# Performance work log

Measured on AMD Instinct MI355X. Metric: run time of the kernel, lower is better.

The kernel has to match this reference:

```python
import jax, jax.numpy as jnp
import numpy as np
import math

MAX_L = 3
N_RBF = 8
CUTOFF = 5.5
P_CUT = 6
ZS = (1, 6, 7, 8)
N_NODES = 10000
N_EDGES = 60000
N_EMB = 3  # n_atom_basis; edge channels = N_EMB**2 = 9


def _lxlylz_list(max_l):
    lst = []
    for l in range(max_l + 1):
        for lx in range(l, -1, -1):
            for ly in range(l - lx, -1, -1):
                lst.append((lx, ly, l - lx - ly))
    return lst

LXLYLZ = _lxlylz_list(MAX_L)            # 20 monomial exponent triples
IDX = {v: i for i, v in enumerate(LXLYLZ)}
L_OF = np.array([sum(v) for v in LXLYLZ], dtype=np.int32)
LX = jnp.array([v[0] for v in LXLYLZ])
LY = jnp.array([v[1] for v in LXLYLZ])
LZ = jnp.array([v[2] for v in LXLYLZ])
L_OF_J = jnp.array(L_OF)
ZS_J = jnp.array(ZS)


def _multinom(v):
    l = sum(v)
    return math.factorial(l) // (math.factorial(v[0]) * math.factorial(v[1]) * math.factorial(v[2]))


def _splits(l):
    return [v for v in LXLYLZ if sum(v) == l]


def _nu2_terms():
    # B2_l = sum_{|lvec|=l} multinom(lvec) * A_lvec^2  (contraction of (r1.r2)^l)
    out = []
    for l in range(1, MAX_L + 1):
        vs = _splits(l)
        idx = jnp.array([IDX[v] for v in vs])
        pref = jnp.array([float(_multinom(v)) for v in vs], dtype=jnp.float32)
        out.append((idx, idx, pref))
    return out


def _nu3_terms():
    # invariants from (r1.r2)^e12 (r1.r3)^e13 (r2.r3)^e23, all e>=1, vector degrees <= MAX_L
    combos = [(a, b, c) for a in range(1, MAX_L + 1) for b in range(1, MAX_L + 1)
              for c in range(1, MAX_L + 1) if a + b <= MAX_L and a + c <= MAX_L and b + c <= MAX_L]
    out = []
    for (e12, e13, e23) in combos:
        coef = {}
        for va in _splits(e12):
            for vb in _splits(e13):
                for vc in _splits(e23):
                    v1 = (va[0] + vb[0], va[1] + vb[1], va[2] + vb[2])
                    v2 = (va[0] + vc[0], va[1] + vc[1], va[2] + vc[2])
                    v3 = (vb[0] + vc[0], vb[1] + vc[1], vb[2] + vc[2])
                    key = (v1, v2, v3)
                    coef[key] = coef.get(key, 0.0) + float(_multinom(va) * _multinom(vb) * _multinom(vc))
        keys = list(coef.keys())
        i1 = jnp.array([IDX[k[0]] for k in keys])
        i2 = jnp.array([IDX[k[1]] for k in keys])
        i3 = jnp.array([IDX[k[2]] for k in keys])
        pref = jnp.array([coef[k] for k in keys], dtype=jnp.float32)
        out.append((i1, i2, i3, pref))
    return out

NU2_TERMS = _nu2_terms()
NU3_TERMS = _nu3_terms()


def setup_inputs() -> dict:
    key = jax.random.key(0)
    k1, k2, k3, k4, k5 = jax.random.split(key, 5)
    positions = jax.random.uniform(k1, (N_NODES, 3), dtype=jnp.float32) * 4.0  # box so most r < cutoff
    atomic_numbers = ZS_J[jax.random.randint(k2, (N_NODES,), 0, len(ZS))]
    edge_index = jax.random.randint(k3, (2, N_EDGES), 0, N_NODES)
    shifts = jnp.zeros((N_EDGES, 3), jnp.float32)
    embedding_weight = jax.random.normal(k4, (len(ZS), N_EMB), jnp.float32) / np.sqrt(len(ZS))
    radial_weight = jax.random.normal(k5, (MAX_L + 1, N_RBF, N_RBF), jnp.float32) / np.sqrt(N_RBF)
    return {"positions": positions, "shifts": shifts, "embedding_weight": embedding_weight,
            "radial_weight": radial_weight, "atomic_numbers": atomic_numbers, "edge_index": edge_index}


def reference(positions, shifts, embedding_weight, radial_weight, atomic_numbers, edge_index):
    # node one-hot + embedding
    onehot = (atomic_numbers[:, None] == ZS_J[None, :]).astype(positions.dtype)
    emb = onehot @ embedding_weight                                   # [N, n_emb]
    snd, rcv = edge_index[0], edge_index[1]
    E = snd.shape[0]
    # directed edge encoding: outer product of endpoint embeddings -> [E, n_emb^2]
    enc = (emb[snd][:, :, None] * emb[rcv][:, None, :]).reshape(E, -1)
    # edge vectors / lengths (normalized)
    vec = positions[rcv] - positions[snd] + shifts
    length = jnp.maximum(jnp.linalg.norm(vec, axis=-1, keepdims=True), 1e-9)  # [E,1]
    unit = vec / length
    # Bessel RBF * polynomial cutoff
    n = jnp.arange(1, N_RBF + 1, dtype=positions.dtype)
    rbf = jnp.sqrt(2.0 / CUTOFF) * jnp.sin(n * jnp.pi * length / CUTOFF) / length  # [E,R]
    x = length / CUTOFF
    p = float(P_CUT)
    fc = (1.0 - 0.5 * (p + 1) * (p + 2) * x ** P_CUT + p * (p + 2) * x ** (P_CUT + 1)
          - 0.5 * p * (p + 1) * x ** (P_CUT + 2)) * (x < 1.0)
    radial = rbf * fc                                                  # [E,R]
    # angular monomials x^lx y^ly z^lz
    pw = unit[:, :, None] ** jnp.arange(MAX_L + 1)                     # [E,3,L+1]
    ang = pw[:, 0, LX] * pw[:, 1, LY] * pw[:, 2, LZ]                   # [E,A=20]
    # triple outer product -> per-edge attribute tensor [E,R,A,C]
    edge_attr = jnp.einsum('er,ea,ec->erac', radial, ang, enc)
    # shared per-l radial linear transform
    Wa = radial_weight[L_OF_J]                                         # [A,R,R]
    edge_attr = jnp.einsum('ars,erac->esac', Wa, edge_attr)
    # scatter-sum to receiver nodes -> A basis
    A = jax.ops.segment_sum(edge_attr, rcv, num_segments=positions.shape[0])  # [N,R,A,C]
    # symmetrizer: invariant B basis up to nu=3
    feats = [A[:, :, 0, :]]                                            # nu=1: A_{000}
    for i1, i2, pref in NU2_TERMS:
        feats.append(jnp.einsum('t,nrtc->nrc', pref, A[:, :, i1, :] * A[:, :, i2, :]))
    for i1, i2, i3, pref in NU3_TERMS:
        feats.append(jnp.einsum('t,nrtc->nrc', pref, A[:, :, i1, :] * A[:, :, i2, :] * A[:, :, i3, :]))
    return jnp.stack(feats, axis=2)                                    # [N, R, n_B=8, C]
```

## Files before the change

### kernel.cpp

```cpp
#include <hip/hip_runtime.h>

constexpr int NRBF = 8;
constexpr int NA   = 20;
constexpr int NC   = 9;
constexpr int EDW  = 64;
constexpr int CAP  = 64;

__constant__ int cLX[NA] = {0,1,0,0,2,1,1,0,0,0,3,2,2,1,1,1,0,0,0,0};
__constant__ int cLY[NA] = {0,0,1,0,0,1,0,2,1,0,0,1,0,2,1,0,3,2,1,0};
__constant__ int cLZ[NA] = {0,0,0,1,0,0,1,0,1,2,0,0,1,0,1,2,0,1,2,3};
__constant__ int cLOF[NA]= {0,1,1,1,2,2,2,2,2,2,3,3,3,3,3,3,3,3,3,3};

__device__ __forceinline__ int zmap(int z) {
    return z == 1 ? 0 : (z == 6 ? 1 : (z == 7 ? 2 : 3));
}

struct Nu3Tbl {
    int n;
    unsigned char i1[200], i2[200], i3[200], cb[200];
    float pref[200];
};
constexpr int idx_of(int lx, int ly, int lz) {
    int l = lx + ly + lz;
    int base = (l == 0) ? 0 : ((l == 1) ? 1 : ((l == 2) ? 4 : 10));
    int d = l - lx;
    return base + d * (d + 1) / 2 + (d - ly);
}
constexpr int factc(int k) { return k <= 1 ? 1 : k * factc(k - 1); }
constexpr float multinom(int lx, int ly, int lz) {
    return (float)(factc(lx + ly + lz) / (factc(lx) * factc(ly) * factc(lz)));
}
constexpr Nu3Tbl make_nu3() {
    Nu3Tbl t{};
    const int combos[4][3] = {{1,1,1},{1,1,2},{1,2,1},{2,1,1}};
    for (int q = 0; q < 4; ++q) {
        int e12 = combos[q][0], e13 = combos[q][1], e23 = combos[q][2];
        for (int ax = e12; ax >= 0; --ax) for (int ay = e12-ax; ay >= 0; --ay) { int az = e12-ax-ay;
        for (int bx = e13; bx >= 0; --bx) for (int by = e13-bx; by >= 0; --by) { int bz = e13-bx-by;
        for (int cx = e23; cx >= 0; --cx) for (int cy = e23-cx; cy >= 0; --cy) { int cz = e23-cx-cy;
            t.i1[t.n] = (unsigned char)idx_of(ax+bx, ay+by, az+bz);
            t.i2[t.n] = (unsigned char)idx_of(ax+cx, ay+cy, az+cz);
            t.i3[t.n] = (unsigned char)idx_of(bx+cx, by+cy, bz+cz);
            t.cb[t.n] = (unsigned char)q;
            t.pref[t.n] = multinom(ax,ay,az) * multinom(bx,by,bz) * multinom(cx,cy,cz);
            t.n++;
        }}}
    }
    return t;
}
constexpr Nu3Tbl NU3 = make_nu3();

__global__ __launch_bounds__(256) void precompute_kernel(
    const float* __restrict__ pos, const float* __restrict__ shifts,
    const float* __restrict__ embW, const float* __restrict__ radW,
    const int* __restrict__ zs, const int* __restrict__ eidx,
    float* __restrict__ edata, int* __restrict__ counts, int* __restrict__ order,
    int E)
{
    __shared__ float s_rad[4][NRBF];
    int w = threadIdx.x >> 6;
    int lane = threadIdx.x & 63;
    int e = blockIdx.x * 4 + w;
    bool valid = (e < E);

    int snd = 0, rcv = 0;
    float dx = 0.f, dy = 0.f, dz = 0.f, len = 1.f;
    if (valid) {
        snd = eidx[e]; rcv = eidx[E + e];
        dx = pos[rcv*3+0] - pos[snd*3+0] + shifts[e*3+0];
        dy = pos[rcv*3+1] - pos[snd*3+1] + shifts[e*3+1];
        dz = pos[rcv*3+2] - pos[snd*3+2] + shifts[e*3+2];
        len = fmaxf(sqrtf(dx*dx + dy*dy + dz*dz), 1e-9f);
    }
    if (valid && lane < 8) {
        float x = len * (1.0f / 5.5f);
        float fc = 0.f;
        if (x < 1.f) {
            float x2 = x * x, x6 = x2 * x2 * x2;
            fc = 1.f - 28.f * x6 + 48.f * x6 * x - 21.f * x6 * x2;
        }
        float rbf = 0.60302268915552724f *
                    sinf((float)(lane + 1) * 3.14159265358979323846f * len / 5.5f) / len;
        s_rad[w][lane] = rbf * fc;
    }
    __syncthreads();
    if (valid) {
        float v = 0.f;
        if (lane < 32) {
            int l = lane >> 3, s = lane & 7;
            float acc = 0.f;
            #pragma unroll
            for (int r = 0; r < 8; ++r) acc += radW[(l * 8 + r) * 8 + s] * s_rad[w][r];
            v = acc;
        } else if (lane < 52) {
            int a = lane - 32;
            float inv = 1.f / len;
            float ux = dx * inv, uy = dy * inv, uz = dz * inv;
            float t = 1.f;
            for (int k = 0; k < cLX[a]; ++k) t *= ux;
            for (int k = 0; k < cLY[a]; ++k) t *= uy;
            for (int k = 0; k < cLZ[a]; ++k) t *= uz;
            v = t;
        } else if (lane < 61) {
            int t = lane - 52;
            v = embW[zmap(zs[snd]) * 3 + t / 3] * embW[zmap(zs[rcv]) * 3 + t % 3];
        }
        edata[(size_t)e * EDW + lane] = v;
        if (lane == 0) {
            int p = atomicAdd(&counts[rcv], 1);
            if (p < CAP) order[rcv * CAP + p] = e;
        }
    }
}

__global__ __launch_bounds__(256) void node_kernel(
    const float* __restrict__ edata, const int* __restrict__ counts,
    const int* __restrict__ order, float* __restrict__ out, int N)
{
    int n = blockIdx.x;
    if (n >= N) return;
    __shared__ float ed[4][EDW];
    __shared__ float A[NRBF * NA * NC];
    __shared__ float Bsh[NRBF * 8 * NC];
    int tid = threadIdx.x;
    int deg = min(counts[n], CAP);

    bool active = (tid < NRBF * NA);
    int s_i = tid / NA, a_i = tid % NA;
    int roff = active ? (cLOF[a_i] * 8 + s_i) : 0;
    int goff = 32 + a_i;
    float acc[NC];
    #pragma unroll
    for (int c = 0; c < NC; ++c) acc[c] = 0.f;

    for (int j = 0; j < deg; j += 4) {
        int slot = tid >> 6, elem = tid & 63;
        if (j + slot < deg)
            ed[slot][elem] = edata[(size_t)order[n * CAP + j + slot] * EDW + elem];
        __syncthreads();
        int m_end = min(4, deg - j);
        for (int m = 0; m < m_end; ++m) {
            if (active) {
                float p = ed[m][roff] * ed[m][goff];
                #pragma unroll
                for (int c = 0; c < NC; ++c) acc[c] += p * ed[m][52 + c];
            }
        }
        __syncthreads();
    }

    if (active) {
        int base = (s_i * NA + a_i) * NC;
        #pragma unroll
        for (int c = 0; c < NC; ++c) A[base + c] = acc[c];
    }
    __syncthreads();

    if (tid < 72) {
        int s = tid / 9, c = tid % 9;
        float Av[NA];
        #pragma unroll
        for (int a = 0; a < NA; ++a) Av[a] = A[(s * NA + a) * NC + c];

        float b0 = Av[0];
        float b1 = Av[1]*Av[1] + Av[2]*Av[2] + Av[3]*Av[3];
        float b2 = Av[4]*Av[4] + 2.f*Av[5]*Av[5] + 2.f*Av[6]*Av[6]
                 + Av[7]*Av[7] + 2.f*Av[8]*Av[8] + Av[9]*Av[9];
        float b3 = Av[10]*Av[10] + 3.f*(Av[11]*Av[11] + Av[12]*Av[12] + Av[13]*Av[13])
                 + 6.f*Av[14]*Av[14] + 3.f*Av[15]*Av[15] + Av[16]*Av[16]
                 + 3.f*(Av[17]*Av[17] + Av[18]*Av[18]) + Av[19]*Av[19];
        float b4 = 0.f, b5 = 0.f, b6 = 0.f, b7 = 0.f;
        #pragma unroll
        for (int k = 0; k < NU3.n; ++k) {
            float term = NU3.pref[k] * Av[NU3.i1[k]] * Av[NU3.i2[k]] * Av[NU3.i3[k]];
            if      (NU3.cb[k] == 0) b4 += term;
            else if (NU3.cb[k] == 1) b5 += term;
            else if (NU3.cb[k] == 2) b6 += term;
            else                     b7 += term;
        }
        int sb = s * 8 * NC + c;
        Bsh[sb + 0*NC] = b0; Bsh[sb + 1*NC] = b1; Bsh[sb + 2*NC] = b2; Bsh[sb + 3*NC] = b3;
        Bsh[sb + 4*NC] = b4; Bsh[sb + 5*NC] = b5; Bsh[sb + 6*NC] = b6; Bsh[sb + 7*NC] = b7;
    }
    __syncthreads();
    float* op = out + (size_t)n * (NRBF * 8 * NC);
    for (int i = tid; i < NRBF * 8 * NC; i += 256) op[i] = Bsh[i];
}

extern "C" void kernel_launch(void* const* d_in, const int* in_sizes, int n_in,
                              void* d_out, int out_size, void* d_ws, size_t ws_size,
                              hipStream_t stream) {
    const float* pos    = (const float*)d_in[0];
    const float* shifts = (const float*)d_in[1];
    const float* embW   = (const float*)d_in[2];
    const float* radW   = (const float*)d_in[3];
    const int*   zs     = (const int*)d_in[4];
    const int*   eidx   = (const int*)d_in[5];
    float* out = (float*)d_out;

    int N = in_sizes[0] / 3;
    int E = in_sizes[5] / 2;

    float* edata = (float*)d_ws;
    int* counts  = (int*)(edata + (size_t)E * EDW);
    int* order   = counts + N;

    hipMemsetAsync(counts, 0, (size_t)N * sizeof(int), stream);

    precompute_kernel<<<dim3((E + 3) / 4), dim3(256), 0, stream>>>(
        pos, shifts, embW, radW, zs, eidx, edata, counts, order, E);

    node_kernel<<<dim3(N), dim3(256), 0, stream>>>(edata, counts, order, out, N);
}
```

Baseline: 134.9 us.

## Remap node kernel threads to (rbf, channel) owning all 20 monomials

The node kernel now assigns each of 72 threads one (radial, channel) pair that accumulates all 20 angular components in registers. This removes the shared-memory A staging and the extra barrier before the symmetrizer. Edges are staged 16 at a time instead of 4, and the block shrinks to 128 threads, which cuts synchronisations and the number of idle threads. In exchange, fewer threads do more serial work per edge and register pressure goes up.

```diff
diff --git a/kernel.cpp b/kernel.cpp
--- a/kernel.cpp
+++ b/kernel.cpp
@@ -5,11 +5,13 @@
 constexpr int NC   = 9;
 constexpr int EDW  = 64;
 constexpr int CAP  = 64;
+constexpr int STG  = 16;
 
 __constant__ int cLX[NA] = {0,1,0,0,2,1,1,0,0,0,3,2,2,1,1,1,0,0,0,0};
 __constant__ int cLY[NA] = {0,0,1,0,0,1,0,2,1,0,0,1,0,2,1,0,3,2,1,0};
 __constant__ int cLZ[NA] = {0,0,0,1,0,0,1,0,1,2,0,0,1,0,1,2,0,1,2,3};
 __constant__ int cLOF[NA]= {0,1,1,1,2,2,2,2,2,2,3,3,3,3,3,3,3,3,3,3};
+constexpr int kLOF[NA]  = {0,1,1,1,2,2,2,2,2,2,3,3,3,3,3,3,3,3,3,3};
 
 __device__ __forceinline__ int zmap(int z) {
     return z == 1 ? 0 : (z == 6 ? 1 : (z == 7 ? 2 : 3));
@@ -113,55 +115,49 @@
     }
 }
 
-__global__ __launch_bounds__(256) void node_kernel(
+__global__ __launch_bounds__(128) void node_kernel(
     const float* __restrict__ edata, const int* __restrict__ counts,
     const int* __restrict__ order, float* __restrict__ out, int N)
 {
     int n = blockIdx.x;
     if (n >= N) return;
-    __shared__ float ed[4][EDW];
-    __shared__ float A[NRBF * NA * NC];
+    __shared__ float ed[STG][EDW];
+    __shared__ int   sidx[STG];
     __shared__ float Bsh[NRBF * 8 * NC];
     int tid = threadIdx.x;
     int deg = min(counts[n], CAP);
 
-    bool active = (tid < NRBF * NA);
-    int s_i = tid / NA, a_i = tid % NA;
-    int roff = active ? (cLOF[a_i] * 8 + s_i) : 0;
-    int goff = 32 + a_i;
-    float acc[NC];
+    bool active = (tid < NRBF * NC);
+    int s_i = tid / NC, c_i = tid % NC;
+
+    float Av[NA];
     #pragma unroll
-    for (int c = 0; c < NC; ++c) acc[c] = 0.f;
-
-    for (int j = 0; j < deg; j += 4) {
-        int slot = tid >> 6, elem = tid & 63;
-        if (j + slot < deg)
-            ed[slot][elem] = edata[(size_t)order[n * CAP + j + slot] * EDW + elem];
+    for (int a = 0; a < NA; ++a) Av[a] = 0.f;
+
+    for (int base = 0; base < deg; base += STG) {
+        int nb = min(STG, deg - base);
+        if (tid < nb) sidx[tid] = order[n * CAP + base + tid];
         __syncthreads();
-        int m_end = min(4, deg - j);
-        for (int m = 0; m < m_end; ++m) {
-            if (active) {
-                float p = ed[m][roff] * ed[m][goff];
+        for (int i = tid; i < nb * EDW; i += 128)
+            ed[i >> 6][i & 63] = edata[(size_t)sidx[i >> 6] * EDW + (i & 63)];
+        __syncthreads();
+        if (active) {
+            for (int m = 0; m < nb; ++m) {
+                float ec = ed[m][52 + c_i];
+                float rl[4];
+                rl[0] = ed[m][ 0 + s_i] * ec;
+                rl[1] = ed[m][ 8 + s_i] * ec;
+                rl[2] = ed[m][16 + s_i] * ec;
+                rl[3] = ed[m][24 + s_i] * ec;
                 #pragma unroll
-                for (int c = 0; c < NC; ++c) acc[c] += p * ed[m][52 + c];
+                for (int a = 0; a < NA; ++a)
+                    Av[a] += rl[kLOF[a]] * ed[m][32 + a];
             }
         }
         __syncthreads();
     }
 
     if (active) {
-        int base = (s_i * NA + a_i) * NC;
-        #pragma unroll
-        for (int c = 0; c < NC; ++c) A[base + c] = acc[c];
-    }
-    __syncthreads();
-
-    if (tid < 72) {
-        int s = tid / 9, c = tid % 9;
-        float Av[NA];
-        #pragma unroll
-        for (int a = 0; a < NA; ++a) Av[a] = A[(s * NA + a) * NC + c];
-
         float b0 = Av[0];
         float b1 = Av[1]*Av[1] + Av[2]*Av[2] + Av[3]*Av[3];
         float b2 = Av[4]*Av[4] + 2.f*Av[5]*Av[5] + 2.f*Av[6]*Av[6]
@@ -178,13 +174,13 @@
             else if (NU3.cb[k] == 2) b6 += term;
             else                     b7 += term;
         }
-        int sb = s * 8 * NC + c;
+        int sb = s_i * 8 * NC + c_i;
         Bsh[sb + 0*NC] = b0; Bsh[sb + 1*NC] = b1; Bsh[sb + 2*NC] = b2; Bsh[sb + 3*NC] = b3;
         Bsh[sb + 4*NC] = b4; Bsh[sb + 5*NC] = b5; Bsh[sb + 6*NC] = b6; Bsh[sb + 7*NC] = b7;
     }
     __syncthreads();
     float* op = out + (size_t)n * (NRBF * 8 * NC);
-    for (int i = tid; i < NRBF * 8 * NC; i += 256) op[i] = Bsh[i];
+    for (int i = tid; i < NRBF * 8 * NC; i += 128) op[i] = Bsh[i];
 }
 
 extern "C" void kernel_launch(void* const* d_in, const int* in_sizes, int n_in,
@@ -210,5 +206,5 @@
     precompute_kernel<<<dim3((E + 3) / 4), dim3(256), 0, stream>>>(
         pos, shifts, embW, radW, zs, eidx, edata, counts, order, E);
 
-    node_kernel<<<dim3(N), dim3(256), 0, stream>>>(edata, counts, order, out, N);
-}
+    node_kernel<<<dim3(N), dim3(128), 0, stream>>>(edata, counts, order, out, N);
+}
```

After: 129.2 us. 4.2% less time.
